# Optimization experiments

Measured on AMD Instinct MI355X. Metric: run time of the kernel, lower is better.

## Reference

```python
import jax, jax.numpy as jnp
import numpy as np

TAU = 0.5
EPS = 1e-12


def _projection(z, W1, b1, W2, b2):
    # fc2(elu(fc1(z)))
    h = jax.nn.elu(z @ W1 + b1)
    return h @ W2 + b2


def _l2_normalize(z):
    n = jnp.linalg.norm(z, axis=1, keepdims=True)
    return z / jnp.maximum(n, EPS)


def _semi_loss(h1, h2, tau):
    n1 = _l2_normalize(h1)
    n2 = _l2_normalize(h2)
    refl = jnp.exp((n1 @ n1.T) / tau)      # [N, N]
    between = jnp.exp((n1 @ n2.T) / tau)   # [N, N]
    denom = refl.sum(axis=1) + between.sum(axis=1) - jnp.diagonal(refl)
    return -jnp.log(jnp.diagonal(between) / denom)


def setup_inputs() -> dict:
    key = jax.random.key(0)
    k1, k2, k3, k4 = jax.random.split(key, 4)
    N, H, P = 12288, 256, 256
    s = 1.0 / np.sqrt(H)
    return {
        "z1": jax.random.normal(k1, (N, H), dtype=jnp.float32),
        "z2": jax.random.normal(k2, (N, H), dtype=jnp.float32),
        "W1": jax.random.normal(k3, (H, P), dtype=jnp.float32) * s,
        "b1": jnp.zeros((P,), dtype=jnp.float32),
        "W2": jax.random.normal(k4, (P, H), dtype=jnp.float32) * s,
        "b2": jnp.zeros((H,), dtype=jnp.float32),
    }


def reference(z1, z2, W1, b1, W2, b2):
    h1 = _projection(z1, W1, b1, W2, b2)
    h2 = _projection(z2, W1, b1, W2, b2)
    l1 = _semi_loss(h1, h2, TAU)
    l2 = _semi_loss(h2, h1, TAU)
    return ((l1 + l2) * 0.5).mean()
```

## Files before the change

### kernel.cpp

```cpp
#include <hip/hip_runtime.h>
#include <hip/hip_bf16.h>

typedef __attribute__((ext_vector_type(4))) float f32x4;
typedef __attribute__((ext_vector_type(8))) short bf16x8;

#define NR 12288
#define HD 256
#define TAU 0.5f
#define NU 24576
#define NTT 192
#define NSUB 384
#define NBLK (NTT * (NTT + 1) / 2)
#define LAM 1.69864368f

__device__ __forceinline__ unsigned short f2bf(float f) {
    unsigned int x = __builtin_bit_cast(unsigned int, f);
    x += 0x7fffu + ((x >> 16) & 1u);
    return (unsigned short)(x >> 16);
}

__device__ __forceinline__ unsigned char f2e4m3(float f) {
    unsigned int u = __builtin_bit_cast(unsigned int, f);
    unsigned int s = (u >> 24) & 0x80u;
    float af = fabsf(f);
    if (af >= 464.f) return (unsigned char)(s | 0x7Eu);
    if (af < 0.015625f) {
        unsigned int q = (unsigned int)(af * 512.f + 0.5f);
        return (unsigned char)(s | q);
    }
    int e = (int)((u >> 23) & 0xffu) - 127;
    unsigned int mant = u & 0x7fffffu;
    unsigned int val = (unsigned int)((e + 7) << 3) | (mant >> 20);
    unsigned int rem = mant & 0xfffffu;
    val += (rem > 0x80000u) || (rem == 0x80000u && (val & 1u));
    return (unsigned char)(s | val);
}

__device__ __forceinline__ float row16_sum(float x) {
    int v;
    v = __builtin_amdgcn_update_dpp(0, __builtin_bit_cast(int, x), 0xB1, 0xF, 0xF, true);
    x += __builtin_bit_cast(float, v);
    v = __builtin_amdgcn_update_dpp(0, __builtin_bit_cast(int, x), 0x4E, 0xF, 0xF, true);
    x += __builtin_bit_cast(float, v);
    v = __builtin_amdgcn_update_dpp(0, __builtin_bit_cast(int, x), 0x141, 0xF, 0xF, true);
    x += __builtin_bit_cast(float, v);
    v = __builtin_amdgcn_update_dpp(0, __builtin_bit_cast(int, x), 0x140, 0xF, 0xF, true);
    x += __builtin_bit_cast(float, v);
    return x;
}

__global__ __launch_bounds__(256) void cast4_kernel(const float* __restrict__ src,
                                                    unsigned short* __restrict__ dst, int n4) {
    int i = blockIdx.x * 256 + threadIdx.x;
    if (i >= n4) return;
    float4 v = ((const float4*)src)[i];
    ushort4 u;
    u.x = f2bf(v.x); u.y = f2bf(v.y); u.z = f2bf(v.z); u.w = f2bf(v.w);
    ((ushort4*)dst)[i] = u;
}

__global__ __launch_bounds__(256) void transpose_cast_kernel(const float* __restrict__ W,
                                                             unsigned short* __restrict__ Wt) {
    int n = blockIdx.x;
    int k = threadIdx.x;
    Wt[n * HD + k] = f2bf(W[k * HD + n]);
}

template <int ELU>
__global__ __launch_bounds__(256) void proj_kernel(const unsigned short* __restrict__ A,
                                                   const unsigned short* __restrict__ Bt,
                                                   const float* __restrict__ bias,
                                                   void* __restrict__ Cout) {
    const int lane = threadIdx.x & 63;
    const int wave = threadIdx.x >> 6;
    const int row0 = blockIdx.x * 64;
    const int col0 = wave * 64;
    const int lr = lane & 15, lk = lane >> 4;

    f32x4 acc[4][4] = {};
    const unsigned short* Ab = A + (size_t)(row0 + lr) * HD + lk * 8;
    const unsigned short* Bb = Bt + (size_t)(col0 + lr) * HD + lk * 8;
#pragma unroll
    for (int k0 = 0; k0 < HD; k0 += 32) {
        bf16x8 af[4], bfr[4];
#pragma unroll
        for (int m = 0; m < 4; ++m) af[m] = *(const bf16x8*)(Ab + m * 16 * HD + k0);
#pragma unroll
        for (int n = 0; n < 4; ++n) bfr[n] = *(const bf16x8*)(Bb + n * 16 * HD + k0);
#pragma unroll
        for (int m = 0; m < 4; ++m)
#pragma unroll
            for (int n = 0; n < 4; ++n)
                acc[m][n] = __builtin_amdgcn_mfma_f32_16x16x32_bf16(af[m], bfr[n], acc[m][n], 0, 0, 0);
    }
#pragma unroll
    for (int m = 0; m < 4; ++m) {
#pragma unroll
        for (int n = 0; n < 4; ++n) {
            int col = col0 + n * 16 + lr;
            float b = bias[col];
#pragma unroll
            for (int r = 0; r < 4; ++r) {
                int row = row0 + m * 16 + lk * 4 + r;
                float v = acc[m][n][r] + b;
                if (ELU) {
                    v = v > 0.f ? v : expm1f(v);
                    ((unsigned short*)Cout)[(size_t)row * HD + col] = f2bf(v);
                } else {
                    ((float*)Cout)[(size_t)row * HD + col] = v;
                }
            }
        }
    }
}

__global__ __launch_bounds__(256) void norm_diag_kernel(const float* __restrict__ h1,
                                                        const float* __restrict__ h2,
                                                        unsigned char* __restrict__ n1,
                                                        unsigned char* __restrict__ n2,
                                                        float* __restrict__ dvec) {
    const int lane = threadIdx.x & 63;
    const int wave = threadIdx.x >> 6;
    const int row = blockIdx.x * 4 + wave;
    const float4 a = *(const float4*)(h1 + (size_t)row * HD + lane * 4);
    const float4 b = *(const float4*)(h2 + (size_t)row * HD + lane * 4);
    float sa = a.x * a.x + a.y * a.y + a.z * a.z + a.w * a.w;
    float sb = b.x * b.x + b.y * b.y + b.z * b.z + b.w * b.w;
    float sab = a.x * b.x + a.y * b.y + a.z * b.z + a.w * b.w;
#pragma unroll
    for (int m = 32; m; m >>= 1) {
        sa += __shfl_xor(sa, m);
        sb += __shfl_xor(sb, m);
        sab += __shfl_xor(sab, m);
    }
    float na = sqrtf(sa); na = na > 1e-12f ? na : 1e-12f;
    float nb = sqrtf(sb); nb = nb > 1e-12f ? nb : 1e-12f;
    float ia = 1.f / na, ib = 1.f / nb;
    float sca = ia * LAM, scb = ib * LAM;
    uchar4 q1, q2;
    q1.x = f2e4m3(a.x * sca); q1.y = f2e4m3(a.y * sca); q1.z = f2e4m3(a.z * sca); q1.w = f2e4m3(a.w * sca);
    q2.x = f2e4m3(b.x * scb); q2.y = f2e4m3(b.y * scb); q2.z = f2e4m3(b.z * scb); q2.w = f2e4m3(b.w * scb);
    const int sw = ((row >> 3) & 1) << 3;
    *(uchar4*)(n1 + (size_t)row * HD + ((lane * 4) ^ sw)) = q1;
    *(uchar4*)(n2 + (size_t)row * HD + ((lane * 4) ^ sw)) = q2;
    if (lane == 0) dvec[row] = sab * ia * ib * (1.f / TAU);
}

__global__ __launch_bounds__(256, 2) void gram_kernel(const unsigned char* __restrict__ nU8,
                                                      float* __restrict__ RPART) {
    __shared__ __align__(16) unsigned char lA[128 * 256];
    __shared__ __align__(16) unsigned char lB[128 * 256];

    const int bid = blockIdx.x;
    const int t0 = (bid & 7) * (NBLK / 8) + (bid >> 3);
    int i = (int)((385.f - sqrtf((float)(385 * 385 - 8 * t0))) * 0.5f);
    if (i < 0) i = 0;
    if (i > NTT - 1) i = NTT - 1;
    while (i > 0 && i * NTT - i * (i - 1) / 2 > t0) --i;
    while ((i + 1) * NTT - (i + 1) * i / 2 <= t0) ++i;
    const int j = i + (t0 - (i * NTT - i * (i - 1) / 2));
    const bool diag = (i == j);

    const unsigned char* X = nU8 + (size_t)i * 128 * HD;
    const unsigned char* Y = nU8 + (size_t)j * 128 * HD;

    const int t = threadIdx.x;
    const int lane = t & 63;
    const int wave = t >> 6;
    const int wr = wave >> 1, wc = wave & 1;
    const int lr = lane & 15, lk = lane >> 4;

    {
        const int rbase = t >> 4;
        const int schunk = (t & 15) ^ rbase;
        const unsigned char* gx = X + rbase * 256 + schunk * 16;
        const unsigned char* gy = Y + rbase * 256 + schunk * 16;
#pragma unroll
        for (int c = 0; c < 8; ++c) {
            __builtin_amdgcn_global_load_lds(
                (const __attribute__((address_space(1))) unsigned int*)(gx + c * 4096),
                (__attribute__((address_space(3))) unsigned int*)(&lA[c * 4096 + t * 16]),
                16, 0, 0);
        }
        if (!diag) {
#pragma unroll
            for (int c = 0; c < 8; ++c) {
                __builtin_amdgcn_global_load_lds(
                    (const __attribute__((address_space(1))) unsigned int*)(gy + c * 4096),
                    (__attribute__((address_space(3))) unsigned int*)(&lB[c * 4096 + t * 16]),
                    16, 0, 0);
            }
        }
    }
    __syncthreads();

    f32x4 acc[4][4] = {};
    const int hswap = (lr >> 3) & 1;
    const unsigned char* sA = lA + (size_t)(wr * 64 + lr) * 256 + ((lk & 1) ^ hswap) * 8;
    const unsigned char* sBb = (diag ? lA : lB);
    const unsigned char* sB = sBb + (size_t)(wc * 64 + lr) * 256 + ((lk & 1) ^ hswap) * 8;

    const unsigned char* pA[8];
    const unsigned char* pB[8];
#pragma unroll
    for (int ks = 0; ks < 8; ++ks) {
        const int chnk = ((2 * ks + (lk >> 1)) ^ lr) * 16;
        pA[ks] = sA + chnk;
        pB[ks] = sB + chnk;
    }

#pragma unroll
    for (int ks = 0; ks < 8; ++ks) {
        long af[4], bfr[4];
#pragma unroll
        for (int m = 0; m < 4; ++m)
            af[m] = *(const long*)(pA[ks] + m * 16 * 256);
#pragma unroll
        for (int n = 0; n < 4; ++n)
            bfr[n] = *(const long*)(pB[ks] + n * 16 * 256);
#pragma unroll
        for (int m = 0; m < 4; ++m)
#pragma unroll
            for (int n = 0; n < 4; ++n)
                acc[m][n] = __builtin_amdgcn_mfma_f32_16x16x32_fp8_fp8(af[m], bfr[n], acc[m][n], 0, 0, 0);
    }

#pragma unroll
    for (int m = 0; m < 4; ++m)
#pragma unroll
        for (int n = 0; n < 4; ++n)
#pragma unroll
            for (int r = 0; r < 4; ++r)
                acc[m][n][r] = exp2f(acc[m][n][r]);

    {
        float* dst = RPART + (size_t)(2 * j + wc) * NU + i * 128 + wr * 64;
#pragma unroll
        for (int m = 0; m < 4; ++m) {
#pragma unroll
            for (int r = 0; r < 4; ++r) {
                float rs = (acc[m][0][r] + acc[m][1][r]) + (acc[m][2][r] + acc[m][3][r]);
                rs = row16_sum(rs);
                if (lr == 0) dst[m * 16 + lk * 4 + r] = rs;
            }
        }
    }
    if (!diag) {
        float* dst = RPART + (size_t)(2 * i + wr) * NU + j * 128 + wc * 64;
#pragma unroll
        for (int n = 0; n < 4; ++n) {
            float cs = 0.f;
#pragma unroll
            for (int m = 0; m < 4; ++m)
#pragma unroll
                for (int r = 0; r < 4; ++r) cs += acc[m][n][r];
            cs += __shfl_xor(cs, 16);
            cs += __shfl_xor(cs, 32);
            if (lk == 0) dst[n * 16 + lr] = cs;
        }
    }
}

__global__ __launch_bounds__(256) void reduce_part_kernel(const float* __restrict__ RPART,
                                                          float* __restrict__ S) {
    const int r = blockIdx.x * 256 + threadIdx.x;
    float s = 0.f;
#pragma unroll 8
    for (int p = 0; p < NSUB; ++p) s += RPART[(size_t)p * NU + r];
    S[r] = s;
}

__global__ __launch_bounds__(128) void loss_partial_kernel(const float* __restrict__ S,
                                                           const float* __restrict__ dvec,
                                                           float* __restrict__ partial) {
    int i = blockIdx.x * 128 + threadIdx.x;
    const float e2 = 7.389056099f;
    float d = dvec[i];
    float l1 = logf(S[i] - e2) - d;
    float l2 = logf(S[NR + i] - e2) - d;
    float v = 0.5f * (l1 + l2);
#pragma unroll
    for (int m = 32; m; m >>= 1) v += __shfl_xor(v, m);
    __shared__ float wsum[2];
    if ((threadIdx.x & 63) == 0) wsum[threadIdx.x >> 6] = v;
    __syncthreads();
    if (threadIdx.x == 0) partial[blockIdx.x] = wsum[0] + wsum[1];
}

__global__ __launch_bounds__(128) void loss_final_kernel(const float* __restrict__ partial,
                                                         float* __restrict__ out, int nb) {
    float s = 0.f;
    for (int i = threadIdx.x; i < nb; i += 128) s += partial[i];
#pragma unroll
    for (int m = 32; m; m >>= 1) s += __shfl_xor(s, m);
    __shared__ float wsum[2];
    if ((threadIdx.x & 63) == 0) wsum[threadIdx.x >> 6] = s;
    __syncthreads();
    if (threadIdx.x == 0) out[0] = (wsum[0] + wsum[1]) * (1.f / (float)NR);
}

extern "C" void kernel_launch(void* const* d_in, const int* in_sizes, int n_in,
                              void* d_out, int out_size, void* d_ws, size_t ws_size,
                              hipStream_t stream) {
    const float* z1 = (const float*)d_in[0];
    const float* z2 = (const float*)d_in[1];
    const float* W1 = (const float*)d_in[2];
    const float* b1 = (const float*)d_in[3];
    const float* W2 = (const float*)d_in[4];
    const float* b2 = (const float*)d_in[5];

    char* ws = (char*)d_ws;
    size_t off = 0;
    auto alloc = [&](size_t bytes) {
        void* p = ws + off;
        off += (bytes + 255) & ~(size_t)255;
        return p;
    };
    const size_t NH2 = (size_t)NR * HD * 2;
    unsigned short* zb1 = (unsigned short*)alloc(NH2);
    unsigned short* zb2 = (unsigned short*)alloc(NH2);
    unsigned short* W1t = (unsigned short*)alloc(HD * HD * 2);
    unsigned short* W2t = (unsigned short*)alloc(HD * HD * 2);
    unsigned short* t1 = (unsigned short*)alloc(NH2);
    unsigned short* t2 = (unsigned short*)alloc(NH2);
    float* h1 = (float*)alloc((size_t)NR * HD * 4);
    float* h2 = (float*)alloc((size_t)NR * HD * 4);
    unsigned char* nU = (unsigned char*)alloc((size_t)NU * HD);
    float* S = (float*)alloc((size_t)NU * 4);
    float* dvec = (float*)alloc(NR * 4);
    float* partial = (float*)alloc(96 * 4);
    float* RPART = (float*)ws;

    const int n4 = NR * HD / 4;
    cast4_kernel<<<(n4 + 255) / 256, 256, 0, stream>>>(z1, zb1, n4);
    cast4_kernel<<<(n4 + 255) / 256, 256, 0, stream>>>(z2, zb2, n4);
    transpose_cast_kernel<<<HD, 256, 0, stream>>>(W1, W1t);
    transpose_cast_kernel<<<HD, 256, 0, stream>>>(W2, W2t);

    proj_kernel<1><<<NR / 64, 256, 0, stream>>>(zb1, W1t, b1, t1);
    proj_kernel<1><<<NR / 64, 256, 0, stream>>>(zb2, W1t, b1, t2);
    proj_kernel<0><<<NR / 64, 256, 0, stream>>>(t1, W2t, b2, h1);
    proj_kernel<0><<<NR / 64, 256, 0, stream>>>(t2, W2t, b2, h2);

    norm_diag_kernel<<<NR / 4, 256, 0, stream>>>(h1, h2, nU, nU + (size_t)NR * HD, dvec);

    gram_kernel<<<NBLK, 256, 0, stream>>>(nU, RPART);

    reduce_part_kernel<<<NU / 256, 256, 0, stream>>>(RPART, S);

    loss_partial_kernel<<<NR / 128, 128, 0, stream>>>(S, dvec, partial);
    loss_final_kernel<<<1, 128, 0, stream>>>(partial, (float*)d_out, NR / 128);
}
```

Baseline: 279.7 us.

## Fuse input casts into projection GEMM and merge launches and reduction kernels

Removes the separate fp32-to-bf16 cast kernels by converting z rows on the fly inside the first projection GEMM. The two transposes and the paired projection launches are batched through blockIdx.y. The partial-sum reduction is also folded into the loss kernel. This cuts launch count and the intermediate bf16 and S buffers. In exchange, the first GEMM reads fp32 inputs directly, doubling its A-operand traffic, and the fused reduction runs with fewer threads (12288 instead of 24576).

```diff
diff --git a/kernel.cpp b/kernel.cpp
--- a/kernel.cpp
+++ b/kernel.cpp
@@ -49,28 +49,36 @@
     return x;
 }
 
-__global__ __launch_bounds__(256) void cast4_kernel(const float* __restrict__ src,
-                                                    unsigned short* __restrict__ dst, int n4) {
-    int i = blockIdx.x * 256 + threadIdx.x;
-    if (i >= n4) return;
-    float4 v = ((const float4*)src)[i];
-    ushort4 u;
-    u.x = f2bf(v.x); u.y = f2bf(v.y); u.z = f2bf(v.z); u.w = f2bf(v.w);
-    ((ushort4*)dst)[i] = u;
-}
-
-__global__ __launch_bounds__(256) void transpose_cast_kernel(const float* __restrict__ W,
-                                                             unsigned short* __restrict__ Wt) {
+__device__ __forceinline__ bf16x8 cvt8(const float* __restrict__ p) {
+    float4 a = *(const float4*)p;
+    float4 b = *(const float4*)(p + 4);
+    union { unsigned int i[4]; bf16x8 v; } u;
+    u.i[0] = ((unsigned int)f2bf(a.y) << 16) | f2bf(a.x);
+    u.i[1] = ((unsigned int)f2bf(a.w) << 16) | f2bf(a.z);
+    u.i[2] = ((unsigned int)f2bf(b.y) << 16) | f2bf(b.x);
+    u.i[3] = ((unsigned int)f2bf(b.w) << 16) | f2bf(b.z);
+    return u.v;
+}
+
+__global__ __launch_bounds__(256) void transpose_cast_kernel(const float* __restrict__ W1,
+                                                             const float* __restrict__ W2,
+                                                             unsigned short* __restrict__ W1t,
+                                                             unsigned short* __restrict__ W2t) {
+    const float* W = blockIdx.y ? W2 : W1;
+    unsigned short* Wt = blockIdx.y ? W2t : W1t;
     int n = blockIdx.x;
     int k = threadIdx.x;
     Wt[n * HD + k] = f2bf(W[k * HD + n]);
 }
 
-template <int ELU>
-__global__ __launch_bounds__(256) void proj_kernel(const unsigned short* __restrict__ A,
-                                                   const unsigned short* __restrict__ Bt,
-                                                   const float* __restrict__ bias,
-                                                   void* __restrict__ Cout) {
+__global__ __launch_bounds__(256) void projA_kernel(const float* __restrict__ z1,
+                                                    const float* __restrict__ z2,
+                                                    const unsigned short* __restrict__ W1t,
+                                                    const float* __restrict__ b1,
+                                                    unsigned short* __restrict__ t1,
+                                                    unsigned short* __restrict__ t2) {
+    const float* A = blockIdx.y ? z2 : z1;
+    unsigned short* C = blockIdx.y ? t2 : t1;
     const int lane = threadIdx.x & 63;
     const int wave = threadIdx.x >> 6;
     const int row0 = blockIdx.x * 64;
@@ -78,13 +86,13 @@
     const int lr = lane & 15, lk = lane >> 4;
 
     f32x4 acc[4][4] = {};
-    const unsigned short* Ab = A + (size_t)(row0 + lr) * HD + lk * 8;
-    const unsigned short* Bb = Bt + (size_t)(col0 + lr) * HD + lk * 8;
+    const unsigned short* Bb = W1t + (size_t)(col0 + lr) * HD + lk * 8;
 #pragma unroll
     for (int k0 = 0; k0 < HD; k0 += 32) {
         bf16x8 af[4], bfr[4];
 #pragma unroll
-        for (int m = 0; m < 4; ++m) af[m] = *(const bf16x8*)(Ab + m * 16 * HD + k0);
+        for (int m = 0; m < 4; ++m)
+            af[m] = cvt8(A + (size_t)(row0 + m * 16 + lr) * HD + k0 + lk * 8);
 #pragma unroll
         for (int n = 0; n < 4; ++n) bfr[n] = *(const bf16x8*)(Bb + n * 16 * HD + k0);
 #pragma unroll
@@ -98,17 +106,58 @@
 #pragma unroll
         for (int n = 0; n < 4; ++n) {
             int col = col0 + n * 16 + lr;
-            float b = bias[col];
+            float b = b1[col];
 #pragma unroll
             for (int r = 0; r < 4; ++r) {
                 int row = row0 + m * 16 + lk * 4 + r;
                 float v = acc[m][n][r] + b;
-                if (ELU) {
-                    v = v > 0.f ? v : expm1f(v);
-                    ((unsigned short*)Cout)[(size_t)row * HD + col] = f2bf(v);
-                } else {
-                    ((float*)Cout)[(size_t)row * HD + col] = v;
-                }
+                v = v > 0.f ? v : expm1f(v);
+                C[(size_t)row * HD + col] = f2bf(v);
+            }
+        }
+    }
+}
+
+__global__ __launch_bounds__(256) void projB_kernel(const unsigned short* __restrict__ t1,
+                                                    const unsigned short* __restrict__ t2,
+                                                    const unsigned short* __restrict__ W2t,
+                                                    const float* __restrict__ b2,
+                                                    float* __restrict__ h1,
+                                                    float* __restrict__ h2) {
+    const unsigned short* A = blockIdx.y ? t2 : t1;
+    float* C = blockIdx.y ? h2 : h1;
+    const int lane = threadIdx.x & 63;
+    const int wave = threadIdx.x >> 6;
+    const int row0 = blockIdx.x * 64;
+    const int col0 = wave * 64;
+    const int lr = lane & 15, lk = lane >> 4;
+
+    f32x4 acc[4][4] = {};
+    const unsigned short* Ab = A + (size_t)(row0 + lr) * HD + lk * 8;
+    const unsigned short* Bb = W2t + (size_t)(col0 + lr) * HD + lk * 8;
+#pragma unroll
+    for (int k0 = 0; k0 < HD; k0 += 32) {
+        bf16x8 af[4], bfr[4];
+#pragma unroll
+        for (int m = 0; m < 4; ++m) af[m] = *(const bf16x8*)(Ab + m * 16 * HD + k0);
+#pragma unroll
+        for (int n = 0; n < 4; ++n) bfr[n] = *(const bf16x8*)(Bb + n * 16 * HD + k0);
+#pragma unroll
+        for (int m = 0; m < 4; ++m)
+#pragma unroll
+            for (int n = 0; n < 4; ++n)
+                acc[m][n] = __builtin_amdgcn_mfma_f32_16x16x32_bf16(af[m], bfr[n], acc[m][n], 0, 0, 0);
+    }
+#pragma unroll
+    for (int m = 0; m < 4; ++m) {
+#pragma unroll
+        for (int n = 0; n < 4; ++n) {
+            int col = col0 + n * 16 + lr;
+            float b = b2[col];
+#pragma unroll
+            for (int r = 0; r < 4; ++r) {
+                int row = row0 + m * 16 + lk * 4 + r;
+                C[(size_t)row * HD + col] = acc[m][n][r] + b;
             }
         }
     }
@@ -261,24 +310,18 @@
     }
 }
 
-__global__ __launch_bounds__(256) void reduce_part_kernel(const float* __restrict__ RPART,
-                                                          float* __restrict__ S) {
-    const int r = blockIdx.x * 256 + threadIdx.x;
-    float s = 0.f;
+__global__ __launch_bounds__(128) void loss_sum_kernel(const float* __restrict__ RPART,
+                                                       const float* __restrict__ dvec,
+                                                       float* __restrict__ partial) {
+    const int i = blockIdx.x * 128 + threadIdx.x;
+    float s1 = 0.f, s2 = 0.f;
 #pragma unroll 8
-    for (int p = 0; p < NSUB; ++p) s += RPART[(size_t)p * NU + r];
-    S[r] = s;
-}
-
-__global__ __launch_bounds__(128) void loss_partial_kernel(const float* __restrict__ S,
-                                                           const float* __restrict__ dvec,
-                                                           float* __restrict__ partial) {
-    int i = blockIdx.x * 128 + threadIdx.x;
+    for (int p = 0; p < NSUB; ++p) {
+        s1 += RPART[(size_t)p * NU + i];
+        s2 += RPART[(size_t)p * NU + NR + i];
+    }
     const float e2 = 7.389056099f;
-    float d = dvec[i];
-    float l1 = logf(S[i] - e2) - d;
-    float l2 = logf(S[NR + i] - e2) - d;
-    float v = 0.5f * (l1 + l2);
+    float v = 0.5f * (logf(s1 - e2) + logf(s2 - e2)) - dvec[i];
 #pragma unroll
     for (int m = 32; m; m >>= 1) v += __shfl_xor(v, m);
     __shared__ float wsum[2];
@@ -317,37 +360,26 @@
         return p;
     };
     const size_t NH2 = (size_t)NR * HD * 2;
-    unsigned short* zb1 = (unsigned short*)alloc(NH2);
-    unsigned short* zb2 = (unsigned short*)alloc(NH2);
+    unsigned short* t1 = (unsigned short*)alloc(NH2);
+    unsigned short* t2 = (unsigned short*)alloc(NH2);
     unsigned short* W1t = (unsigned short*)alloc(HD * HD * 2);
     unsigned short* W2t = (unsigned short*)alloc(HD * HD * 2);
-    unsigned short* t1 = (unsigned short*)alloc(NH2);
-    unsigned short* t2 = (unsigned short*)alloc(NH2);
     float* h1 = (float*)alloc((size_t)NR * HD * 4);
     float* h2 = (float*)alloc((size_t)NR * HD * 4);
     unsigned char* nU = (unsigned char*)alloc((size_t)NU * HD);
-    float* S = (float*)alloc((size_t)NU * 4);
     float* dvec = (float*)alloc(NR * 4);
     float* partial = (float*)alloc(96 * 4);
     float* RPART = (float*)ws;
 
-    const int n4 = NR * HD / 4;
-    cast4_kernel<<<(n4 + 255) / 256, 256, 0, stream>>>(z1, zb1, n4);
-    cast4_kernel<<<(n4 + 255) / 256, 256, 0, stream>>>(z2, zb2, n4);
-    transpose_cast_kernel<<<HD, 256, 0, stream>>>(W1, W1t);
-    transpose_cast_kernel<<<HD, 256, 0, stream>>>(W2, W2t);
-
-    proj_kernel<1><<<NR / 64, 256, 0, stream>>>(zb1, W1t, b1, t1);
-    proj_kernel<1><<<NR / 64, 256, 0, stream>>>(zb2, W1t, b1, t2);
-    proj_kernel<0><<<NR / 64, 256, 0, stream>>>(t1, W2t, b2, h1);
-    proj_kernel<0><<<NR / 64, 256, 0, stream>>>(t2, W2t, b2, h2);
+    transpose_cast_kernel<<<dim3(HD, 2), 256, 0, stream>>>(W1, W2, W1t, W2t);
+
+    projA_kernel<<<dim3(NR / 64, 2), 256, 0, stream>>>(z1, z2, W1t, b1, t1, t2);
+    projB_kernel<<<dim3(NR / 64, 2), 256, 0, stream>>>(t1, t2, W2t, b2, h1, h2);
 
     norm_diag_kernel<<<NR / 4, 256, 0, stream>>>(h1, h2, nU, nU + (size_t)NR * HD, dvec);
 
     gram_kernel<<<NBLK, 256, 0, stream>>>(nU, RPART);
 
-    reduce_part_kernel<<<NU / 256, 256, 0, stream>>>(RPART, S);
-
-    loss_partial_kernel<<<NR / 128, 128, 0, stream>>>(S, dvec, partial);
+    loss_sum_kernel<<<NR / 128, 128, 0, stream>>>(RPART, dvec, partial);
     loss_final_kernel<<<1, 128, 0, stream>>>(partial, (float*)d_out, NR / 128);
 }
```

Measured after the change: 275.5 us. About the same (-1.5%).
